# Kernel tuning notes

Hardware: AMD Instinct MI355X
Metric: run time of the kernel (lower is better)

The kernel has to match this reference:

```python
import jax, jax.numpy as jnp
import numpy as np

N = 100000
E = 1600000
VOCAB = 16
D = 128   # node_embedding_dim == hidden_channels
NUM_LAYERS = 3


def setup_inputs() -> dict:
    key = jax.random.key(0)
    ks = jax.random.split(key, 12)
    x = jax.random.randint(ks[0], (N, 1), 0, VOCAB, dtype=jnp.int64) if jax.config.jax_enable_x64 else jax.random.randint(ks[0], (N, 1), 0, VOCAB, dtype=jnp.int32)
    edge_index = jax.random.randint(ks[1], (2, E), 0, N, dtype=jnp.int32)
    s = 1.0 / np.sqrt(D)
    inp = {
        "x": x,
        "edge_index": edge_index,
        "emb": jax.random.normal(ks[2], (VOCAB, D), jnp.float32),
        "W0": jax.random.normal(ks[3], (D, D), jnp.float32) * s,
        "b0": jnp.zeros((D,), jnp.float32),
        "W1": jax.random.normal(ks[4], (D, D), jnp.float32) * s,
        "b1": jnp.zeros((D,), jnp.float32),
        "W2": jax.random.normal(ks[5], (D, D), jnp.float32) * s,
        "b2": jnp.zeros((D,), jnp.float32),
        "Wm1": jax.random.normal(ks[6], (2 * D, D), jnp.float32) * (1.0 / np.sqrt(2 * D)),
        "bm1": jnp.zeros((D,), jnp.float32),
        "Wm2": jax.random.normal(ks[7], (D, 3), jnp.float32) * s,
        "bm2": jnp.zeros((3,), jnp.float32),
    }
    return inp


def _gcn_conv(h, src_sl, dst_sl, norm, W, b):
    # PyG GCNConv: x' = scatter_dst(norm * (x W)[src]) + b, with self-loops included
    hW = h @ W                                   # [N, D]
    msg = hW[src_sl] * norm[:, None]             # [(E+N), D] gather
    agg = jax.ops.segment_sum(msg, dst_sl, num_segments=N)  # scatter-add
    return agg + b


def reference(x, edge_index, emb, W0, b0, W1, b1, W2, b2, Wm1, bm1, Wm2, bm2):
    src, dst = edge_index[0], edge_index[1]
    # add self-loops
    loop = jnp.arange(N, dtype=src.dtype)
    src_sl = jnp.concatenate([src, loop])
    dst_sl = jnp.concatenate([dst, loop])
    # symmetric degree normalization: deg counted on dst (col)
    deg = jax.ops.segment_sum(jnp.ones_like(dst_sl, jnp.float32), dst_sl, num_segments=N)
    dis = jnp.where(deg > 0, jax.lax.rsqrt(jnp.maximum(deg, 1.0)), 0.0)
    norm = dis[src_sl] * dis[dst_sl]             # [(E+N)]

    # node encoder: embedding lookup (dropout omitted: eval mode)
    h = emb[x[:, 0]]                             # [N, D]
    for W, b in ((W0, b0), (W1, b1), (W2, b2)):
        h = jax.nn.relu(_gcn_conv(h, src_sl, dst_sl, norm, W, b))

    # edge classifier: gather endpoints, concat, MLP
    ef = jnp.concatenate([h[src], h[dst]], axis=-1)   # [E, 2D]
    hid = jax.nn.relu(ef @ Wm1 + bm1)
    return hid @ Wm2 + bm2                             # [E, 3]
```

## Files before the change

### kernel.cpp

```cpp
#include <hip/hip_runtime.h>
#include <hip/hip_bf16.h>

#define N_NODES 100000
#define N_EDGES 1600000


__global__ void zero_cnt_k(int* cnt, int n) {
    int i = blockIdx.x * 256 + threadIdx.x;
    if (i < n) cnt[i] = 0;
}

__global__ void hist_k(const int* __restrict__ ei, int* __restrict__ cnt, int E) {
    int e = blockIdx.x * 256 + threadIdx.x;
    if (e < E) atomicAdd(&cnt[ei[E + e]], 1);
}

__global__ void dis_k(const int* __restrict__ cnt, const int* __restrict__ x,
                      float* __restrict__ dis, float2* __restrict__ sx, int n) {
    int i = blockIdx.x * 256 + threadIdx.x;
    if (i < n) {
        float d = rsqrtf(1.0f + (float)cnt[i]);
        dis[i] = d;
        sx[i] = make_float2(d, __int_as_float(x[i]));
    }
}

__global__ void scan_cnt_k(const int* __restrict__ cnt, int* __restrict__ offs,
                           int* __restrict__ bsum, int n) {
    __shared__ int buf[2][256];
    int t = threadIdx.x;
    int i = blockIdx.x * 256 + t;
    int v = (i < n) ? cnt[i] : 0;
    int p = 0;
    buf[0][t] = v;
    __syncthreads();
    for (int off = 1; off < 256; off <<= 1) {
        int nv = buf[p][t];
        if (t >= off) nv += buf[p][t - off];
        buf[p ^ 1][t] = nv;
        p ^= 1;
        __syncthreads();
    }
    if (i < n) offs[i] = buf[p][t] - v;
    if (t == 255) bsum[blockIdx.x] = buf[p][t];
}

__global__ void scan_bsum_k(int* __restrict__ bsum, int nb) {
    __shared__ int buf[2][512];
    int t = threadIdx.x;
    int v = (t < nb) ? bsum[t] : 0;
    int p = 0;
    buf[0][t] = v;
    __syncthreads();
    for (int off = 1; off < 512; off <<= 1) {
        int nv = buf[p][t];
        if (t >= off) nv += buf[p][t - off];
        buf[p ^ 1][t] = nv;
        p ^= 1;
        __syncthreads();
    }
    if (t < nb) bsum[t] = buf[p][t] - v;
}

__global__ void scan_add_k(int* __restrict__ offs, int* __restrict__ cursor,
                           const int* __restrict__ bsum, int n, int total) {
    int i = blockIdx.x * 256 + threadIdx.x;
    if (i < n) {
        int o = offs[i] + bsum[blockIdx.x];
        offs[i] = o;
        cursor[i] = o;
    }
    if (i == 0) offs[n] = total;
}

__global__ void fill_csr_k(const int* __restrict__ ei, int* __restrict__ cursor,
                           int2* __restrict__ se, int E) {
    int e = blockIdx.x * 256 + threadIdx.x;
    if (e < E) {
        int s = ei[e];
        int d = ei[E + e];
        int pos = atomicAdd(&cursor[d], 1);
        se[pos] = make_int2(s, e);
    }
}


__global__ void t0_k(const float* __restrict__ emb, const float* __restrict__ W0,
                     float* __restrict__ T0) {
    int v = blockIdx.x;
    int c = threadIdx.x;
    float acc = 0.f;
    for (int k = 0; k < 128; ++k) acc += emb[v * 128 + k] * W0[k * 128 + c];
    T0[v * 128 + c] = acc;
}

__global__ __launch_bounds__(256) void vgather_k(const float2* __restrict__ sx,
                                                 const int* __restrict__ offs,
                                                 const int2* __restrict__ se,
                                                 const float* __restrict__ dis,
                                                 const int* __restrict__ x,
                                                 const float* __restrict__ T0,
                                                 const float* __restrict__ b0,
                                                 float* __restrict__ h, int n) {
    __shared__ float t0s[16 * 128];
    __shared__ float cv[4][16];
    int t = threadIdx.x;
    #pragma unroll
    for (int i = 0; i < 8; ++i) t0s[t + i * 256] = T0[t + i * 256];
    if (t < 64) cv[t >> 4][t & 15] = 0.f;
    __syncthreads();

    int w = t >> 6, lane = t & 63;
    int node = blockIdx.x * 4 + w;
    float di = dis[node];
    int j0 = offs[node], j1 = offs[node + 1];
    for (int j = j0 + lane; j < j1; j += 64) {
        int s = se[j].x;
        float2 v = sx[s];
        atomicAdd(&cv[w][__float_as_int(v.y)], v.x);
    }
    if (lane == 0) atomicAdd(&cv[w][x[node]], di);
    __syncthreads();

    float2 acc = make_float2(0.f, 0.f);
    #pragma unroll
    for (int v = 0; v < 16; ++v) {
        float c = cv[w][v];
        float2 tv = *(const float2*)&t0s[v * 128 + lane * 2];
        acc.x += c * tv.x;
        acc.y += c * tv.y;
    }
    float2 bb = *(const float2*)&b0[lane * 2];
    float2 r = make_float2(fmaxf(di * acc.x + bb.x, 0.f),
                           fmaxf(di * acc.y + bb.y, 0.f));
    ((float2*)h)[(size_t)node * 64 + lane] = r;
}


__global__ __launch_bounds__(256) void matmul128_k(const float* __restrict__ in,
                                                   const float* __restrict__ W,
                                                   float* __restrict__ out,
                                                   const float* __restrict__ scale,
                                                   int n) {
    __shared__ float hlds[64][132];
    int t = threadIdx.x;
    int row0 = blockIdx.x * 64;
    #pragma unroll
    for (int it = 0; it < 8; ++it) {
        int i4 = t + it * 256;
        int r = i4 >> 5, c4 = (i4 & 31) << 2;
        float4 v = make_float4(0.f, 0.f, 0.f, 0.f);
        int g = row0 + r;
        if (g < n) v = *(const float4*)&in[(size_t)g * 128 + c4];
        *(float4*)&hlds[r][c4] = v;
    }
    __syncthreads();
    int cg = t & 31, rg = t >> 5;
    int c0 = cg << 2;
    float acc[8][4];
    #pragma unroll
    for (int r = 0; r < 8; ++r)
        for (int j = 0; j < 4; ++j) acc[r][j] = 0.f;
    #pragma unroll 4
    for (int k = 0; k < 128; ++k) {
        float4 w = *(const float4*)&W[(size_t)k * 128 + c0];
        #pragma unroll
        for (int r = 0; r < 8; ++r) {
            float hk = hlds[rg * 8 + r][k];
            acc[r][0] += hk * w.x;
            acc[r][1] += hk * w.y;
            acc[r][2] += hk * w.z;
            acc[r][3] += hk * w.w;
        }
    }
    #pragma unroll
    for (int r = 0; r < 8; ++r) {
        int g = row0 + rg * 8 + r;
        if (g < n) {
            float sc = scale ? scale[g] : 1.0f;
            float4 o = make_float4(acc[r][0] * sc, acc[r][1] * sc,
                                   acc[r][2] * sc, acc[r][3] * sc);
            *(float4*)&out[(size_t)g * 128 + c0] = o;
        }
    }
}

__global__ void gcn_gather_k(const float* __restrict__ hW, const int* __restrict__ offs,
                             const int2* __restrict__ se, const float* __restrict__ dis,
                             const float* __restrict__ bias, float* __restrict__ hout,
                             int n) {
    int node = blockIdx.x * 4 + (threadIdx.x >> 6);
    int lane = threadIdx.x & 63;
    float di = dis[node];
    const float2* hw2 = (const float2*)hW;
    float2 acc = hw2[(size_t)node * 64 + lane];
    int j1 = offs[node + 1];
    for (int j = offs[node]; j < j1; ++j) {
        int s = se[j].x;
        float2 u = hw2[(size_t)s * 64 + lane];
        acc.x += u.x;
        acc.y += u.y;
    }
    float2 bb = *(const float2*)&bias[lane * 2];
    float2 r = make_float2(fmaxf(di * acc.x + bb.x, 0.f),
                           fmaxf(di * acc.y + bb.y, 0.f));
    ((float2*)hout)[(size_t)node * 64 + lane] = r;
}

__global__ __launch_bounds__(256) void edge_mlp_k(const int* __restrict__ offs,
                                                  const int2* __restrict__ se,
                                                  const float* __restrict__ A,
                                                  const float* __restrict__ B,
                                                  const float* __restrict__ Wm2,
                                                  const float* __restrict__ bm1,
                                                  const float* __restrict__ bm2,
                                                  float* __restrict__ out, int n) {
    int t = threadIdx.x;
    int node = blockIdx.x * 4 + (t >> 6);
    int lane = t & 63;
    int g = lane >> 4, sl = lane & 15;
    int j0 = offs[node], j1 = offs[node + 1];
    if (j0 == j1) return;

    const float4* B4 = (const float4*)(B + (size_t)node * 128 + sl * 8);
    const float4* bm14 = (const float4*)(bm1 + sl * 8);
    float4 pre0 = B4[0], pre1 = B4[1];
    float4 m0 = bm14[0], m1 = bm14[1];
    pre0.x += m0.x; pre0.y += m0.y; pre0.z += m0.z; pre0.w += m0.w;
    pre1.x += m1.x; pre1.y += m1.y; pre1.z += m1.z; pre1.w += m1.w;

    float wv[8][3];
    #pragma unroll
    for (int i = 0; i < 8; ++i) {
        int f = sl * 8 + i;
        wv[i][0] = Wm2[f * 3 + 0];
        wv[i][1] = Wm2[f * 3 + 1];
        wv[i][2] = Wm2[f * 3 + 2];
    }
    float c0 = bm2[0], c1 = bm2[1], c2 = bm2[2];

    for (int jb = j0; jb < j1; jb += 4) {
        int jj = jb + g;
        bool act = jj < j1;
        int2 se_ = se[act ? jj : j0];
        int s = se_.x, e = se_.y;
        const float4* A4 = (const float4*)(A + (size_t)s * 128 + sl * 8);
        float4 a0 = A4[0], a1 = A4[1];
        float h[8];
        h[0] = fmaxf(a0.x + pre0.x, 0.f);
        h[1] = fmaxf(a0.y + pre0.y, 0.f);
        h[2] = fmaxf(a0.z + pre0.z, 0.f);
        h[3] = fmaxf(a0.w + pre0.w, 0.f);
        h[4] = fmaxf(a1.x + pre1.x, 0.f);
        h[5] = fmaxf(a1.y + pre1.y, 0.f);
        h[6] = fmaxf(a1.z + pre1.z, 0.f);
        h[7] = fmaxf(a1.w + pre1.w, 0.f);
        float p0 = 0.f, p1 = 0.f, p2 = 0.f;
        #pragma unroll
        for (int i = 0; i < 8; ++i) {
            p0 += h[i] * wv[i][0];
            p1 += h[i] * wv[i][1];
            p2 += h[i] * wv[i][2];
        }
        #pragma unroll
        for (int m = 1; m <= 8; m <<= 1) {
            p0 += __shfl_xor(p0, m);
            p1 += __shfl_xor(p1, m);
            p2 += __shfl_xor(p2, m);
        }
        if (act && sl == 0) {
            out[(size_t)e * 3 + 0] = p0 + c0;
            out[(size_t)e * 3 + 1] = p1 + c1;
            out[(size_t)e * 3 + 2] = p2 + c2;
        }
    }
}

extern "C" void kernel_launch(void* const* d_in, const int* in_sizes, int n_in,
                              void* d_out, int out_size, void* d_ws, size_t ws_size,
                              hipStream_t stream) {
    const int N = N_NODES, E = N_EDGES;
    const int* x    = (const int*)d_in[0];
    const int* ei   = (const int*)d_in[1];
    const float* emb = (const float*)d_in[2];
    const float* W0 = (const float*)d_in[3];
    const float* b0 = (const float*)d_in[4];
    const float* W1 = (const float*)d_in[5];
    const float* b1 = (const float*)d_in[6];
    const float* W2 = (const float*)d_in[7];
    const float* b2 = (const float*)d_in[8];
    const float* Wm1 = (const float*)d_in[9];
    const float* bm1 = (const float*)d_in[10];
    const float* Wm2 = (const float*)d_in[11];
    const float* bm2 = (const float*)d_in[12];
    float* out = (float*)d_out;

    char* p = (char*)d_ws;
    auto alloc = [&](size_t bytes) {
        char* r = p;
        p += (bytes + 511) & ~(size_t)511;
        return r;
    };
    int*    cnt    = (int*)alloc((size_t)N * 4);
    float*  dis    = (float*)alloc((size_t)N * 4);
    float2* sx     = (float2*)alloc((size_t)N * 8);
    int*    offs   = (int*)alloc((size_t)(N + 1) * 4);
    int*    cursor = (int*)alloc((size_t)N * 4);
    int*    bsum   = (int*)alloc(512 * 4);
    int2*   se     = (int2*)alloc((size_t)E * 8);
    float*  T0     = (float*)alloc(16 * 128 * 4);
    float*  buf0   = (float*)alloc((size_t)N * 128 * 4);
    float*  buf1   = (float*)alloc((size_t)N * 128 * 4);
    float*  buf2   = (float*)alloc((size_t)N * 128 * 4);

    int nbN = (N + 255) / 256;
    int nbE = (E + 255) / 256;
    int nodeBlocks = N / 4;
    int mmBlocks = (N + 63) / 64;

    zero_cnt_k<<<nbN, 256, 0, stream>>>(cnt, N);
    hist_k<<<nbE, 256, 0, stream>>>(ei, cnt, E);
    dis_k<<<nbN, 256, 0, stream>>>(cnt, x, dis, sx, N);
    scan_cnt_k<<<nbN, 256, 0, stream>>>(cnt, offs, bsum, N);
    scan_bsum_k<<<1, 512, 0, stream>>>(bsum, nbN);
    scan_add_k<<<nbN, 256, 0, stream>>>(offs, cursor, bsum, N, E);
    fill_csr_k<<<nbE, 256, 0, stream>>>(ei, cursor, se, E);

    t0_k<<<16, 128, 0, stream>>>(emb, W0, T0);
    vgather_k<<<nodeBlocks, 256, 0, stream>>>(sx, offs, se, dis, x, T0, b0, buf0, N);

    const float* Ws[2] = {W1, W2};
    const float* bs[2] = {b1, b2};
    for (int l = 0; l < 2; ++l) {
        matmul128_k<<<mmBlocks, 256, 0, stream>>>(buf0, Ws[l], buf1, dis, N);
        gcn_gather_k<<<nodeBlocks, 256, 0, stream>>>(buf1, offs, se, dis, bs[l], buf0, N);
    }

    matmul128_k<<<mmBlocks, 256, 0, stream>>>(buf0, Wm1, buf1, nullptr, N);
    matmul128_k<<<mmBlocks, 256, 0, stream>>>(buf0, Wm1 + 128 * 128, buf2, nullptr, N);

    edge_mlp_k<<<nodeBlocks, 256, 0, stream>>>(offs, se, buf1, buf2, Wm2, bm1, bm2, out, N);
}
```

Baseline: 928.8 us.

## Split CSR into SoA arrays, parallelize gather over edges, fuse MLP matmuls

The interleaved (src, edge id) CSR array is split into separate src and edge-id arrays, so the gather kernels read only the 4-byte sources they need. The GCN gather now has each wave handle four neighbours at once with float4 loads per 16-lane group, then combines the partial sums with cross-lane shuffles, which exposes more memory-level parallelism per node. The two edge-MLP first-layer matmuls are fused into one kernel that loads the node features once and produces both halves. The cost is extra accumulator registers in the fused matmul, which may lower occupancy, and reduction overhead in the gather.

```diff
diff --git a/kernel.cpp b/kernel.cpp
--- a/kernel.cpp
+++ b/kernel.cpp
@@ -74,13 +74,14 @@
 }
 
 __global__ void fill_csr_k(const int* __restrict__ ei, int* __restrict__ cursor,
-                           int2* __restrict__ se, int E) {
+                           int* __restrict__ srcs, int* __restrict__ eid, int E) {
     int e = blockIdx.x * 256 + threadIdx.x;
     if (e < E) {
         int s = ei[e];
         int d = ei[E + e];
         int pos = atomicAdd(&cursor[d], 1);
-        se[pos] = make_int2(s, e);
+        srcs[pos] = s;
+        eid[pos] = e;
     }
 }
 
@@ -96,7 +97,7 @@
 
 __global__ __launch_bounds__(256) void vgather_k(const float2* __restrict__ sx,
                                                  const int* __restrict__ offs,
-                                                 const int2* __restrict__ se,
+                                                 const int* __restrict__ srcs,
                                                  const float* __restrict__ dis,
                                                  const int* __restrict__ x,
                                                  const float* __restrict__ T0,
@@ -115,8 +116,7 @@
     float di = dis[node];
     int j0 = offs[node], j1 = offs[node + 1];
     for (int j = j0 + lane; j < j1; j += 64) {
-        int s = se[j].x;
-        float2 v = sx[s];
+        float2 v = sx[srcs[j]];
         atomicAdd(&cv[w][__float_as_int(v.y)], v.x);
     }
     if (lane == 0) atomicAdd(&cv[w][x[node]], di);
@@ -177,7 +177,7 @@
     for (int r = 0; r < 8; ++r) {
         int g = row0 + rg * 8 + r;
         if (g < n) {
-            float sc = scale ? scale[g] : 1.0f;
+            float sc = scale[g];
             float4 o = make_float4(acc[r][0] * sc, acc[r][1] * sc,
                                    acc[r][2] * sc, acc[r][3] * sc);
             *(float4*)&out[(size_t)g * 128 + c0] = o;
@@ -185,30 +185,109 @@
     }
 }
 
-__global__ void gcn_gather_k(const float* __restrict__ hW, const int* __restrict__ offs,
-                             const int2* __restrict__ se, const float* __restrict__ dis,
-                             const float* __restrict__ bias, float* __restrict__ hout,
-                             int n) {
-    int node = blockIdx.x * 4 + (threadIdx.x >> 6);
-    int lane = threadIdx.x & 63;
-    float di = dis[node];
-    const float2* hw2 = (const float2*)hW;
-    float2 acc = hw2[(size_t)node * 64 + lane];
-    int j1 = offs[node + 1];
-    for (int j = offs[node]; j < j1; ++j) {
-        int s = se[j].x;
-        float2 u = hw2[(size_t)s * 64 + lane];
-        acc.x += u.x;
-        acc.y += u.y;
-    }
-    float2 bb = *(const float2*)&bias[lane * 2];
-    float2 r = make_float2(fmaxf(di * acc.x + bb.x, 0.f),
-                           fmaxf(di * acc.y + bb.y, 0.f));
-    ((float2*)hout)[(size_t)node * 64 + lane] = r;
+__global__ __launch_bounds__(256) void matmulAB_k(const float* __restrict__ in,
+                                                  const float* __restrict__ WA,
+                                                  const float* __restrict__ WB,
+                                                  float* __restrict__ outA,
+                                                  float* __restrict__ outB, int n) {
+    __shared__ float hlds[64][132];
+    int t = threadIdx.x;
+    int row0 = blockIdx.x * 64;
+    #pragma unroll
+    for (int it = 0; it < 8; ++it) {
+        int i4 = t + it * 256;
+        int r = i4 >> 5, c4 = (i4 & 31) << 2;
+        float4 v = make_float4(0.f, 0.f, 0.f, 0.f);
+        int g = row0 + r;
+        if (g < n) v = *(const float4*)&in[(size_t)g * 128 + c4];
+        *(float4*)&hlds[r][c4] = v;
+    }
+    __syncthreads();
+    int cg = t & 31, rg = t >> 5;
+    int c0 = cg << 2;
+    float accA[8][4], accB[8][4];
+    #pragma unroll
+    for (int r = 0; r < 8; ++r)
+        for (int j = 0; j < 4; ++j) { accA[r][j] = 0.f; accB[r][j] = 0.f; }
+    #pragma unroll 2
+    for (int k = 0; k < 128; ++k) {
+        float4 wa = *(const float4*)&WA[(size_t)k * 128 + c0];
+        float4 wb = *(const float4*)&WB[(size_t)k * 128 + c0];
+        #pragma unroll
+        for (int r = 0; r < 8; ++r) {
+            float hk = hlds[rg * 8 + r][k];
+            accA[r][0] += hk * wa.x;
+            accA[r][1] += hk * wa.y;
+            accA[r][2] += hk * wa.z;
+            accA[r][3] += hk * wa.w;
+            accB[r][0] += hk * wb.x;
+            accB[r][1] += hk * wb.y;
+            accB[r][2] += hk * wb.z;
+            accB[r][3] += hk * wb.w;
+        }
+    }
+    #pragma unroll
+    for (int r = 0; r < 8; ++r) {
+        int g = row0 + rg * 8 + r;
+        if (g < n) {
+            *(float4*)&outA[(size_t)g * 128 + c0] = *(float4*)&accA[r][0];
+            *(float4*)&outB[(size_t)g * 128 + c0] = *(float4*)&accB[r][0];
+        }
+    }
+}
+
+__global__ __launch_bounds__(256) void gcn_gather_k(const float* __restrict__ hW,
+                                                    const int* __restrict__ offs,
+                                                    const int* __restrict__ srcs,
+                                                    const float* __restrict__ dis,
+                                                    const float* __restrict__ bias,
+                                                    float* __restrict__ hout, int n) {
+    int t = threadIdx.x;
+    int node = blockIdx.x * 4 + (t >> 6);
+    int lane = t & 63;
+    int g = lane >> 4, sl = lane & 15;
+    const float4* hw4 = (const float4*)hW;
+    float4 a0 = make_float4(0.f, 0.f, 0.f, 0.f), a1 = a0;
+    if (g == 0) {
+        size_t rb = (size_t)node * 32 + sl * 2;
+        a0 = hw4[rb];
+        a1 = hw4[rb + 1];
+    }
+    int j0 = offs[node], j1 = offs[node + 1];
+    for (int j = j0 + g; j < j1; j += 4) {
+        size_t rb = (size_t)srcs[j] * 32 + sl * 2;
+        float4 u0 = hw4[rb], u1 = hw4[rb + 1];
+        a0.x += u0.x; a0.y += u0.y; a0.z += u0.z; a0.w += u0.w;
+        a1.x += u1.x; a1.y += u1.y; a1.z += u1.z; a1.w += u1.w;
+    }
+    #pragma unroll
+    for (int m = 16; m <= 32; m <<= 1) {
+        a0.x += __shfl_xor(a0.x, m); a0.y += __shfl_xor(a0.y, m);
+        a0.z += __shfl_xor(a0.z, m); a0.w += __shfl_xor(a0.w, m);
+        a1.x += __shfl_xor(a1.x, m); a1.y += __shfl_xor(a1.y, m);
+        a1.z += __shfl_xor(a1.z, m); a1.w += __shfl_xor(a1.w, m);
+    }
+    if (g == 0) {
+        float di = dis[node];
+        float4 bb0 = *(const float4*)&bias[sl * 8];
+        float4 bb1 = *(const float4*)&bias[sl * 8 + 4];
+        float4 r0 = make_float4(fmaxf(di * a0.x + bb0.x, 0.f),
+                                fmaxf(di * a0.y + bb0.y, 0.f),
+                                fmaxf(di * a0.z + bb0.z, 0.f),
+                                fmaxf(di * a0.w + bb0.w, 0.f));
+        float4 r1 = make_float4(fmaxf(di * a1.x + bb1.x, 0.f),
+                                fmaxf(di * a1.y + bb1.y, 0.f),
+                                fmaxf(di * a1.z + bb1.z, 0.f),
+                                fmaxf(di * a1.w + bb1.w, 0.f));
+        size_t rb = (size_t)node * 32 + sl * 2;
+        ((float4*)hout)[rb] = r0;
+        ((float4*)hout)[rb + 1] = r1;
+    }
 }
 
 __global__ __launch_bounds__(256) void edge_mlp_k(const int* __restrict__ offs,
-                                                  const int2* __restrict__ se,
+                                                  const int* __restrict__ srcs,
+                                                  const int* __restrict__ eid,
                                                   const float* __restrict__ A,
                                                   const float* __restrict__ B,
                                                   const float* __restrict__ Wm2,
@@ -242,8 +321,9 @@
     for (int jb = j0; jb < j1; jb += 4) {
         int jj = jb + g;
         bool act = jj < j1;
-        int2 se_ = se[act ? jj : j0];
-        int s = se_.x, e = se_.y;
+        int jsafe = act ? jj : j0;
+        int s = srcs[jsafe];
+        int e = eid[jsafe];
         const float4* A4 = (const float4*)(A + (size_t)s * 128 + sl * 8);
         float4 a0 = A4[0], a1 = A4[1];
         float h[8];
@@ -307,7 +387,8 @@
     int*    offs   = (int*)alloc((size_t)(N + 1) * 4);
     int*    cursor = (int*)alloc((size_t)N * 4);
     int*    bsum   = (int*)alloc(512 * 4);
-    int2*   se     = (int2*)alloc((size_t)E * 8);
+    int*    srcs   = (int*)alloc((size_t)E * 4);
+    int*    eid    = (int*)alloc((size_t)E * 4);
     float*  T0     = (float*)alloc(16 * 128 * 4);
     float*  buf0   = (float*)alloc((size_t)N * 128 * 4);
     float*  buf1   = (float*)alloc((size_t)N * 128 * 4);
@@ -324,20 +405,19 @@
     scan_cnt_k<<<nbN, 256, 0, stream>>>(cnt, offs, bsum, N);
     scan_bsum_k<<<1, 512, 0, stream>>>(bsum, nbN);
     scan_add_k<<<nbN, 256, 0, stream>>>(offs, cursor, bsum, N, E);
-    fill_csr_k<<<nbE, 256, 0, stream>>>(ei, cursor, se, E);
+    fill_csr_k<<<nbE, 256, 0, stream>>>(ei, cursor, srcs, eid, E);
 
     t0_k<<<16, 128, 0, stream>>>(emb, W0, T0);
-    vgather_k<<<nodeBlocks, 256, 0, stream>>>(sx, offs, se, dis, x, T0, b0, buf0, N);
+    vgather_k<<<nodeBlocks, 256, 0, stream>>>(sx, offs, srcs, dis, x, T0, b0, buf0, N);
 
     const float* Ws[2] = {W1, W2};
     const float* bs[2] = {b1, b2};
     for (int l = 0; l < 2; ++l) {
         matmul128_k<<<mmBlocks, 256, 0, stream>>>(buf0, Ws[l], buf1, dis, N);
-        gcn_gather_k<<<nodeBlocks, 256, 0, stream>>>(buf1, offs, se, dis, bs[l], buf0, N);
-    }
-
-    matmul128_k<<<mmBlocks, 256, 0, stream>>>(buf0, Wm1, buf1, nullptr, N);
-    matmul128_k<<<mmBlocks, 256, 0, stream>>>(buf0, Wm1 + 128 * 128, buf2, nullptr, N);
-
-    edge_mlp_k<<<nodeBlocks, 256, 0, stream>>>(offs, se, buf1, buf2, Wm2, bm1, bm2, out, N);
-}
+        gcn_gather_k<<<nodeBlocks, 256, 0, stream>>>(buf1, offs, srcs, dis, bs[l], buf0, N);
+    }
+
+    matmulAB_k<<<mmBlocks, 256, 0, stream>>>(buf0, Wm1, Wm1 + 128 * 128, buf1, buf2, N);
+
+    edge_mlp_k<<<nodeBlocks, 256, 0, stream>>>(offs, srcs, eid, buf1, buf2, Wm2, bm1, bm2, out, N);
+}
```

Result: faster. 819.9 us (-11.7%).
